# Performance work log

Hardware: AMD Instinct MI355X
Metric: run time of the kernel (lower is better)

The kernel has to match this reference:

```python
import jax, jax.numpy as jnp
import numpy as np

B, T, N, D = 4, 24, 5000, 64
M, K = 256, 20
TEMP = 0.5
MASK_T = int(T * 0.2)


def _random_walk(A):
    # D^-1 A with inf -> 0, as in calculate_random_walk_matrix
    deg = A.sum(axis=1)
    d_inv = jnp.where(deg > 0, 1.0 / deg, 0.0)
    return d_inv[:, None] * A


def _gnn(h, S1, S2, W, b):
    # SpatialConvOrderK, order=1, support_len=2, include_self=True
    # h: [B, C, N, T]; diffusion along node axis; 1x1 conv == channel matmul
    m1 = jnp.einsum('bcnt,mn->bcmt', h, S1)
    m2 = jnp.einsum('bcnt,mn->bcmt', h, S2)
    hc = jnp.concatenate([h, m1, m2], axis=1)  # [B, 3C, N, T]
    return jnp.einsum('bcnt,cd->bdnt', hc, W) + b[None, :, None, None]


def _encode(x, S1, S2, W_start, b_start, W1, b1, W2, b2):
    h = x @ W_start + b_start                 # [B, T, N, D]
    h = jnp.transpose(h, (0, 3, 2, 1))        # [B, D, N, T]
    h = jax.nn.relu(_gnn(h, S1, S2, W1, b1))
    h = _gnn(h, S1, S2, W2, b2)
    return h                                  # [B, D, N, T]


def _normalize(z):
    # cosine-similarity normalization over channel axis (dim=1), torch eps=1e-8
    n = jnp.sqrt(jnp.sum(z * z, axis=1, keepdims=True))
    return z / jnp.maximum(n, 1e-8)


def _forward(x, adj, W_start, b_start, W1, b1, W2, b2, Wf1, bf1, Wf2, bf2,
             missing_idx, pos_idx, neg_idx):
    S1 = _random_walk(adj)
    S2 = _random_walk(adj.T)
    h_ori = _encode(x, S1, S2, W_start, b_start, W1, b1, W2, b2)
    # augmented view: time-masked input through the same encoder
    x_aug = x.at[:, :MASK_T].set(0.0)
    h_aug = _encode(x_aug, S1, S2, W_start, b_start, W1, b1, W2, b2)
    # imputation head: final_linear1 -> relu -> final_linear2
    ht = jnp.transpose(h_ori, (0, 3, 2, 1))   # [B, T, N, D]
    y = jax.nn.relu(ht @ Wf1 + bf1) @ Wf2 + bf2  # [B, T, N, 1]
    # vectorized RSCL: batched gather + cosine sim + InfoNCE (label 0 = positive)
    Zo = _normalize(jnp.transpose(h_ori, (0, 1, 3, 2)))  # [B, D, T, N]
    Za = _normalize(jnp.transpose(h_aug, (0, 1, 3, 2)))
    anchor = Zo[..., missing_idx]             # [B, D, T, M]
    pos = Za[..., pos_idx]                    # [B, D, T, M]
    neg = Za[..., neg_idx]                    # [B, D, T, M, K]
    pos_sim = jnp.sum(anchor * pos, axis=1)                  # [B, T, M]
    neg_sim = jnp.einsum('bdtm,bdtmk->btmk', anchor, neg)    # [B, T, M, K]
    logits = jnp.concatenate([pos_sim[..., None], neg_sim], axis=-1) / TEMP
    # cross-entropy with label 0 == logsumexp - positive logit
    loss = jnp.mean(jax.nn.logsumexp(logits, axis=-1) - logits[..., 0])
    return y, loss


def setup_inputs() -> dict:
    key = jax.random.key(0)
    ks = jax.random.split(key, 12)
    x = jax.random.normal(ks[0], (B, T, N, 1), jnp.float32)
    adj = jax.random.uniform(ks[1], (N, N), jnp.float32)
    missing_idx = jax.random.randint(ks[2], (M,), 0, N)
    pos_idx = jax.random.randint(ks[3], (M,), 0, N)
    neg_idx = jax.random.randint(ks[4], (M, K), 0, N)
    s = lambda k, shp, fan: (jax.random.normal(k, shp, jnp.float32) / np.sqrt(fan)).astype(jnp.float32)
    W_start = s(ks[5], (1, D), 1.0)
    b_start = jnp.zeros((D,), jnp.float32)
    W1 = s(ks[6], (3 * D, D), 3.0 * D)
    b1 = jnp.zeros((D,), jnp.float32)
    W2 = s(ks[7], (3 * D, D), 3.0 * D)
    b2 = jnp.zeros((D,), jnp.float32)
    Wf1 = s(ks[8], (D, D // 2), float(D))
    bf1 = jnp.zeros((D // 2,), jnp.float32)
    Wf2 = s(ks[9], (D // 2, 1), float(D // 2))
    bf2 = jnp.zeros((1,), jnp.float32)
    return dict(x=x, adj=adj, W_start=W_start, b_start=b_start, W1=W1, b1=b1,
                W2=W2, b2=b2, Wf1=Wf1, bf1=bf1, Wf2=Wf2, bf2=bf2,
                missing_idx=missing_idx, pos_idx=pos_idx, neg_idx=neg_idx)


def reference(x, adj, W_start, b_start, W1, b1, W2, b2, Wf1, bf1, Wf2, bf2,
              missing_idx, pos_idx, neg_idx):
    return _forward(x, adj, W_start, b_start, W1, b1, W2, b2, Wf1, bf1, Wf2, bf2,
                    missing_idx, pos_idx, neg_idx)
```

## Files before the change

### kernel.cpp

```cpp
#include <hip/hip_runtime.h>

typedef unsigned char u8;
typedef unsigned short u16;
typedef unsigned int u32;
typedef __attribute__((ext_vector_type(8))) short short8;
typedef __attribute__((ext_vector_type(8))) u16 u16x8;
typedef __attribute__((ext_vector_type(4))) float f32x4;
typedef __attribute__((ext_vector_type(4))) int i32x4;
typedef __attribute__((ext_vector_type(8))) int i32x8;

#define N_NODES 5000
#define NP 5120
#define BTOT 96
#define J_DIM 6144
#define TT 24
#define KNEG 20

__device__ __forceinline__ float b2f(u16 u){ union{u32 i; float f;} x; x.i = ((u32)u)<<16; return x.f; }
__device__ __forceinline__ u16 f2b(float f){ union{float fl; u32 i;} x; x.fl = f; u32 r = (x.i + 0x7fffu + ((x.i>>16)&1u))>>16; return (u16)r; }
__device__ __forceinline__ u8 f2e4(float f){ return (u8)(__builtin_amdgcn_cvt_pk_fp8_f32(f, 0.f, 0, false) & 0xff); }

#define GPERM(r) ((((r)>>1)&3) | (((r)&1)<<2))
#define GLOAD16(g, l) __builtin_amdgcn_global_load_lds((const __attribute__((address_space(1))) void*)(g), (__attribute__((address_space(3))) void*)(l), 16, 0, 0)

__global__ void k_prep(const float* __restrict__ Ws, const float* __restrict__ bs,
                       const float* __restrict__ W1, const float* __restrict__ b1,
                       const float* __restrict__ W2, const float* __restrict__ b2,
                       float* __restrict__ consts, u16* __restrict__ w2t)
{
  int d = threadIdx.x;
  float u0=0.f,u1=0.f,u2=0.f,bb=0.f;
  for (int c=0;c<64;c++){
    float w = Ws[c];
    float a = W1[c*64+d], b_ = W1[(64+c)*64+d], cw = W1[(128+c)*64+d];
    u0 += w*a; u1 += w*b_; u2 += w*cw;
    bb += bs[c]*(a+b_+cw);
  }
  bb += b1[d];
  consts[d]=u0; consts[64+d]=u1; consts[128+d]=u2; consts[192+d]=bb;
  __shared__ float rb[64];
  rb[d] = fmaxf(bb, 0.f);
  __syncthreads();
  float cA=0.f,cB=0.f,cC=0.f;
  for (int c=0;c<64;c++){
    float r = rb[c];
    cA += r*W2[c*64+d]; cB += r*W2[(64+c)*64+d]; cC += r*W2[(128+c)*64+d];
  }
  consts[256+d]=cA; consts[320+d]=cB; consts[384+d]=cC;
  for (int c=0;c<192;c++) w2t[d*192 + c] = f2b(W2[c*64 + d]);
  __syncthreads();
  float b2v = b2[d];
  for (int vi=0; vi<4; vi++){
    float vv = cA + ((vi&1) ? cB : 0.f) + ((vi&2) ? cC : 0.f) + b2v;
    rb[d] = vv*vv;
    __syncthreads();
    for (int o=32;o;o>>=1){ if (d<o) rb[d]+=rb[d+o]; __syncthreads(); }
    float nrm = sqrtf(rb[0]);
    consts[448 + vi*64 + d] = vv / fmaxf(nrm, 1e-8f);
    __syncthreads();
  }
}

__global__ __launch_bounds__(256) void k_convT(const float* __restrict__ adj,
    u8* __restrict__ abf, u8* __restrict__ atbf,
    float* __restrict__ degr, float* __restrict__ degc)
{
  __shared__ u8 tN[64][80];
  __shared__ u8 tT[64][80];
  __shared__ float rsum[64];
  __shared__ float cpart[16][64];
  const int tid = threadIdx.x;
  const int bx = blockIdx.x, by = blockIdx.y;
  const int c4 = (tid & 15) * 4;
  const int g  = tid >> 4;
  const int gk = bx*64 + c4;
  float ca0=0.f, ca1=0.f, ca2=0.f, ca3=0.f;
  #pragma unroll
  for (int p=0;p<4;p++){
    int r = p*16 + g;
    int gm = by*64 + r;
    float v0=0.f,v1=0.f,v2=0.f,v3=0.f;
    if (gm < N_NODES && gk + 3 < N_NODES){
      const float4 v = *(const float4*)(adj + (size_t)gm*N_NODES + gk);
      v0=v.x; v1=v.y; v2=v.z; v3=v.w;
    }
    u8 p0=f2e4(v0), p1=f2e4(v1), p2=f2e4(v2), p3=f2e4(v3);
    *(u32*)&tN[r][c4] = (u32)p0 | ((u32)p1<<8) | ((u32)p2<<16) | ((u32)p3<<24);
    tT[c4+0][r]=p0; tT[c4+1][r]=p1; tT[c4+2][r]=p2; tT[c4+3][r]=p3;
    float ls = v0+v1+v2+v3;
    ls += __shfl_xor(ls,1); ls += __shfl_xor(ls,2);
    ls += __shfl_xor(ls,4); ls += __shfl_xor(ls,8);
    if ((tid & 15) == 0) rsum[r] = ls;
    ca0+=v0; ca1+=v1; ca2+=v2; ca3+=v3;
  }
  cpart[g][c4+0]=ca0; cpart[g][c4+1]=ca1; cpart[g][c4+2]=ca2; cpart[g][c4+3]=ca3;
  __syncthreads();
  if (tid < 64){
    int gm = by*64 + tid;
    if (gm < N_NODES && rsum[tid] != 0.f) atomicAdd(&degr[gm], rsum[tid]);
    float cs = 0.f;
    #pragma unroll
    for (int gg=0;gg<16;gg++) cs += cpart[gg][tid];
    int gc = bx*64 + tid;
    if (gc < N_NODES && cs != 0.f) atomicAdd(&degc[gc], cs);
  }
  const int j = tid >> 2, c16 = (tid & 3) * 16;
  *(i32x4*)(abf  + (size_t)(by*64+j)*NP + bx*64 + c16) = *(const i32x4*)(&tN[j][c16]);
  *(i32x4*)(atbf + (size_t)(bx*64+j)*NP + by*64 + c16) = *(const i32x4*)(&tT[j][c16]);
}

__global__ void k_xbf(const float* __restrict__ x, u8* __restrict__ xbf){
  int i4 = (blockIdx.x*256 + threadIdx.x)*4;
  int j = i4 / NP, n = i4 - j*NP;
  u32 w = 0;
  if (j < BTOT){
    #pragma unroll
    for (int e=0;e<4;e++){
      float v = (n+e < N_NODES) ? x[(size_t)j*N_NODES + n + e] : 0.f;
      w |= ((u32)f2e4(v)) << (8*e);
    }
  }
  *(u32*)(xbf + i4) = w;
}

__device__ __forceinline__ i32x8 frag8(const u8* lds, int row, int kb2){
  int g = GPERM(row & 7);
  int ba = row*128 + ((kb2 ^ g)<<4);
  union { i32x8 v; i32x4 h[2]; } f;
  f.h[0] = *(const i32x4*)(lds + ba);
  f.h[1] = *(const i32x4*)(lds + (ba^16));
  return f.v;
}

__global__ __launch_bounds__(256) void k_sgemm8(const u8* __restrict__ abf,
    const u8* __restrict__ atbf, const u8* __restrict__ B,
    float* __restrict__ y1sl, float* __restrict__ y2sl)
{
  __shared__ __align__(16) u8 lA[2][16384];
  __shared__ __align__(16) u8 lB[2][16384];
  const u8* A = blockIdx.z ? atbf : abf;
  float* ysl = blockIdx.z ? y2sl : y1sl;
  const int tid = threadIdx.x, lane = tid & 63, wv = tid >> 6;
  const int wm = (wv >> 1) * 64, wj = (wv & 1) * 64;
  const int m0 = blockIdx.x * 128;
  const int kbase = blockIdx.y * 640;
  f32x4 acc[4][4] = {};
  const int q = tid >> 3;
  const int sc = ((tid & 7) ^ GPERM(q & 7)) << 4;
  const u8* gA = A + (size_t)(m0 + q)*NP + kbase + sc;
  const u8* gB = B + (size_t)q*NP + kbase + sc;

  #define SSTAGE8(k0, bufA, bufB) do { \
    _Pragma("unroll") \
    for (int s=0;s<4;s++){ \
      GLOAD16(gA + (size_t)(s*32)*NP + (k0), (char*)(bufA) + s*4096 + wv*1024); \
      GLOAD16(gB + (size_t)(s*32)*NP + (k0), (char*)(bufB) + s*4096 + wv*1024); \
    } \
  } while(0)

  SSTAGE8(0,   lA[0], lB[0]);
  SSTAGE8(128, lA[1], lB[1]);
  asm volatile("s_waitcnt vmcnt(8)" ::: "memory");
  __builtin_amdgcn_s_barrier();
  __builtin_amdgcn_sched_barrier(0);

  for (int t = 0; t < 5; t++) {
    const int cur = t & 1;
    const u8* bA = lA[cur];
    const u8* bB = lB[cur];
    i32x8 af[4], bfv[4];
    const int kb2 = (lane >> 4) * 2;
    #pragma unroll
    for (int i=0;i<4;i++){
      af[i]  = frag8(bA, wm + i*16 + (lane&15), kb2);
      bfv[i] = frag8(bB, wj + i*16 + (lane&15), kb2);
    }
    __builtin_amdgcn_s_setprio(1);
    #pragma unroll
    for (int i=0;i<4;i++)
      #pragma unroll
      for (int j=0;j<4;j++)
        acc[i][j] = __builtin_amdgcn_mfma_scale_f32_16x16x128_f8f6f4(
            af[i], bfv[j], acc[i][j], 0, 0, 0, 0x7f7f7f7f, 0, 0x7f7f7f7f);
    __builtin_amdgcn_s_setprio(0);
    __builtin_amdgcn_s_barrier();
    __builtin_amdgcn_sched_barrier(0);
    if (t + 2 < 5) {
      SSTAGE8((t+2)*128, lA[cur], lB[cur]);
      asm volatile("s_waitcnt vmcnt(8)" ::: "memory");
    } else {
      asm volatile("s_waitcnt vmcnt(0)" ::: "memory");
    }
    __builtin_amdgcn_s_barrier();
    __builtin_amdgcn_sched_barrier(0);
  }
  #undef SSTAGE8

  float* yb = ysl + (size_t)blockIdx.y * NP * 128;
  #pragma unroll
  for (int i=0;i<4;i++)
    #pragma unroll
    for (int r=0;r<4;r++){
      int row = m0 + wm + i*16 + (lane>>4)*4 + r;
      #pragma unroll
      for (int j=0;j<4;j++){
        int col = wj + j*16 + (lane&15);
        yb[(size_t)row*128 + col] = acc[i][j][r];
      }
    }
}

__global__ __launch_bounds__(256) void k_yred(const float* __restrict__ y1sl,
    const float* __restrict__ y2sl, const float* __restrict__ degr,
    const float* __restrict__ degc, float* __restrict__ y1r, float* __restrict__ y2r)
{
  __shared__ float tb[128][66];
  const int n0 = blockIdx.x*64;
  const int bt = threadIdx.x & 127, nh = threadIdx.x >> 7;
  const int nl = threadIdx.x & 63, bh = threadIdx.x >> 6;
  #pragma unroll 4
  for (int k=0;k<32;k++){
    int n = nh*32 + k;
    float s = 0.f;
    #pragma unroll
    for (int sl=0; sl<8; sl++) s += y1sl[((size_t)sl*NP + n0+n)*128 + bt];
    tb[bt][n] = s;
  }
  __syncthreads();
  {
    float dv = degr[n0+nl];
    float iv = (dv > 0.f) ? 1.f/dv : 0.f;
    #pragma unroll 4
    for (int b=0;b<32;b++){
      int btw = bh*32 + b;
      y1r[(size_t)btw*NP + n0 + nl] = iv * tb[btw][nl];
    }
  }
  __syncthreads();
  #pragma unroll 4
  for (int k=0;k<32;k++){
    int n = nh*32 + k;
    float s = 0.f;
    #pragma unroll
    for (int sl=0; sl<8; sl++) s += y2sl[((size_t)sl*NP + n0+n)*128 + bt];
    tb[bt][n] = s;
  }
  __syncthreads();
  {
    float dv = degc[n0+nl];
    float iv = (dv > 0.f) ? 1.f/dv : 0.f;
    #pragma unroll 4
    for (int b=0;b<32;b++){
      int btw = bh*32 + b;
      y2r[(size_t)btw*NP + n0 + nl] = iv * tb[btw][nl];
    }
  }
}

__global__ __launch_bounds__(256) void k_h1(const float* __restrict__ x,
    const float* __restrict__ y1r, const float* __restrict__ y2r,
    const float* __restrict__ consts, u8* __restrict__ h1t, u16* __restrict__ h1n)
{
  __shared__ u8 trT[64][80];
  const int tid = threadIdx.x;
  const int n = tid & 63, d0 = (tid >> 6) * 16;
  const int n0 = blockIdx.x * 64;
  const int bt = blockIdx.y;
  const int gn = n0 + n;
  const bool valid = gn < N_NODES;
  float xv  = valid ? x[(size_t)bt*N_NODES + gn] : 0.f;
  float y1s = y1r[(size_t)bt*NP + gn];
  float y2s = y2r[(size_t)bt*NP + gn];
  float hv[16];
  #pragma unroll
  for (int e=0;e<16;e++){
    int d = d0 + e;
    float v = 0.f;
    if (valid)
      v = fmaxf(xv*consts[d] + y1s*consts[64+d] + y2s*consts[128+d] + consts[192+d], 0.f);
    hv[e] = v;
    trT[d][n] = f2e4(v);
  }
  u16x8 p0, p1;
  #pragma unroll
  for (int e=0;e<8;e++){ p0[e]=f2b(hv[e]); p1[e]=f2b(hv[8+e]); }
  u16* dst = h1n + (size_t)gn*J_DIM + bt*64 + d0;
  *(u16x8*)dst = p0;
  *(u16x8*)(dst+8) = p1;
  __syncthreads();
  const int d = tid >> 2, c16 = (tid & 3) * 16;
  *(i32x4*)(h1t + (size_t)(bt*64+d)*NP + n0 + c16) = *(const i32x4*)(&trT[d][c16]);
}

__global__ __launch_bounds__(512, 2) void k_gemm8(
    const u8* __restrict__ abf, const u8* __restrict__ atbf,
    const u8* __restrict__ Bt, u16* __restrict__ Pb, u16* __restrict__ Qb,
    const float* __restrict__ degr, const float* __restrict__ degc)
{
  __shared__ __align__(16) u8 lA[2][32768];
  __shared__ __align__(16) u8 lB[2][32768];
  const u8* A = blockIdx.z ? atbf : abf;
  u16* C = blockIdx.z ? Qb : Pb;
  const float* dg = blockIdx.z ? degc : degr;
  const int tid = threadIdx.x, lane = tid & 63, wv = tid >> 6;
  const int wm = (wv >> 1) * 64;
  const int wn = (wv & 1) * 128;
  const int m0 = blockIdx.x * 256;
  const int j0 = blockIdx.y * 256;
  f32x4 acc[4][8] = {};
  const int q = tid >> 3;
  const int sc = ((tid & 7) ^ GPERM(q & 7)) << 4;
  const u8* gA = A + (size_t)(m0 + q)*NP + sc;
  const u8* gB = Bt + (size_t)(j0 + q)*NP + sc;

  #define STAGE8(k0, bufA, bufB) do { \
    _Pragma("unroll") \
    for (int s=0;s<4;s++){ \
      GLOAD16(gA + (size_t)(s*64)*NP + (k0), (char*)(bufA) + s*8192 + wv*1024); \
      GLOAD16(gB + (size_t)(s*64)*NP + (k0), (char*)(bufB) + s*8192 + wv*1024); \
    } \
  } while(0)

  STAGE8(0,   lA[0], lB[0]);
  STAGE8(128, lA[1], lB[1]);
  asm volatile("s_waitcnt vmcnt(8)" ::: "memory");
  __builtin_amdgcn_s_barrier();
  __builtin_amdgcn_sched_barrier(0);

  const int NT = NP/128;
  for (int t = 0; t < NT; t++) {
    const int cur = t & 1;
    const u8* bA = lA[cur];
    const u8* bB = lB[cur];
    const int kb2 = (lane >> 4) * 2;
    const int rl = lane & 15;
    i32x8 af[4];
    #pragma unroll
    for (int i=0;i<4;i++) af[i] = frag8(bA, wm + i*16 + rl, kb2);
    __builtin_amdgcn_s_setprio(1);
    #pragma unroll
    for (int j=0;j<8;j++){
      i32x8 bf = frag8(bB, wn + j*16 + rl, kb2);
      #pragma unroll
      for (int i=0;i<4;i++)
        acc[i][j] = __builtin_amdgcn_mfma_scale_f32_16x16x128_f8f6f4(
            af[i], bf, acc[i][j], 0, 0, 0, 0x7f7f7f7f, 0, 0x7f7f7f7f);
    }
    __builtin_amdgcn_s_setprio(0);
    __builtin_amdgcn_s_barrier();
    __builtin_amdgcn_sched_barrier(0);
    if (t + 2 < NT) {
      STAGE8((t+2)*128, lA[cur], lB[cur]);
      asm volatile("s_waitcnt vmcnt(8)" ::: "memory");
    } else {
      asm volatile("s_waitcnt vmcnt(0)" ::: "memory");
    }
    __builtin_amdgcn_s_barrier();
    __builtin_amdgcn_sched_barrier(0);
  }
  #undef STAGE8

  #pragma unroll
  for (int i=0;i<4;i++)
    #pragma unroll
    for (int r=0;r<4;r++){
      int row = m0 + wm + i*16 + (lane>>4)*4 + r;
      float dv = dg[row];
      float scl = (dv > 0.f) ? 1.f/dv : 0.f;
      #pragma unroll
      for (int j=0;j<8;j++){
        int col = j0 + wn + j*16 + (lane&15);
        C[(size_t)row*J_DIM + col] = f2b(acc[i][j][r] * scl);
      }
    }
}

__global__ __launch_bounds__(256) void k_comb(const u16* __restrict__ h1n,
  const u16* __restrict__ P, const u16* __restrict__ Q,
  const u16* __restrict__ w2t, const float* __restrict__ b2,
  const float* __restrict__ Wf1, const float* __restrict__ bf1,
  const float* __restrict__ Wf2, const float* __restrict__ bf2,
  u16* __restrict__ horin, float* __restrict__ yout)
{
  __shared__ float w1L[64*33];
  __shared__ float hT[64][65];
  __shared__ float b1L[32], w2Ls[32];
  const int tid = threadIdx.x;
  for (int i = tid; i < 2048; i += 256) w1L[(i>>5)*33 + (i&31)] = Wf1[i];
  if (tid < 32){ b1L[tid] = bf1[tid]; w2Ls[tid] = Wf2[tid]; }
  const int lane = tid & 63;
  const int wv = tid >> 6;
  const int n0 = blockIdx.x * 64 + wv * 16;
  const int bt = blockIdx.y;
  const int rl = lane & 15, kh = lane >> 4;

  f32x4 acc[4] = {};
  const size_t rowoff = (size_t)(n0 + rl) * J_DIM + bt*64;
  const u16* bases[3] = { h1n + rowoff, P + rowoff, Q + rowoff };
  #pragma unroll
  for (int s=0;s<3;s++){
    const u16* base = bases[s];
    #pragma unroll
    for (int kk=0;kk<2;kk++){
      short8 af = *(const short8*)(base + kk*32 + kh*8);
      #pragma unroll
      for (int j=0;j<4;j++){
        short8 bf = *(const short8*)(w2t + (j*16+rl)*192 + s*64 + kk*32 + kh*8);
        acc[j] = __builtin_amdgcn_mfma_f32_16x16x32_bf16(af, bf, acc[j], 0,0,0);
      }
    }
  }
  float hvv[4][4];
  #pragma unroll
  for (int j=0;j<4;j++){
    float bias = b2[j*16 + rl];
    #pragma unroll
    for (int r=0;r<4;r++) hvv[j][r] = acc[j][r] + bias;
  }
  float inv[4];
  #pragma unroll
  for (int r=0;r<4;r++){
    float s = hvv[0][r]*hvv[0][r] + hvv[1][r]*hvv[1][r]
            + hvv[2][r]*hvv[2][r] + hvv[3][r]*hvv[3][r];
    s += __shfl_xor(s,1); s += __shfl_xor(s,2);
    s += __shfl_xor(s,4); s += __shfl_xor(s,8);
    inv[r] = 1.f / fmaxf(sqrtf(s), 1e-8f);
  }
  #pragma unroll
  for (int j=0;j<4;j++){
    int d = j*16 + rl;
    #pragma unroll
    for (int r=0;r<4;r++){
      int nn = n0 + kh*4 + r;
      hT[wv*16 + kh*4 + r][d] = hvv[j][r];
      if (nn < N_NODES)
        horin[((size_t)bt*N_NODES + nn)*64 + d] = f2b(hvv[j][r] * inv[r]);
    }
  }
  __syncthreads();
  const int qd = tid & 3, node = tid >> 2;
  float h[16];
  #pragma unroll
  for (int e=0;e<16;e++) h[e] = hT[node][qd*16 + e];
  float yacc = 0.f;
  #pragma unroll
  for (int jj=0; jj<32; jj++){
    float s = 0.f;
    #pragma unroll
    for (int dl=0; dl<16; dl++) s += h[dl]*w1L[(qd*16+dl)*33 + jj];
    s += __shfl_xor(s, 1);
    s += __shfl_xor(s, 2);
    s += b1L[jj];
    yacc += fmaxf(s, 0.f)*w2Ls[jj];
  }
  int gn = blockIdx.x*64 + node;
  if (qd == 0 && gn < N_NODES)
    yout[(size_t)bt*N_NODES + gn] = yacc + bf2[0];
}

__global__ __launch_bounds__(256) void k_loss(const u16* __restrict__ horin,
  const int* __restrict__ missing, const int* __restrict__ posi, const int* __restrict__ negi,
  const float* __restrict__ degr, const float* __restrict__ degc,
  const float* __restrict__ consts, float* __restrict__ out)
{
  const int lane = threadIdx.x & 63;
  const int wv = threadIdx.x >> 6;
  const int wg = blockIdx.x*4 + wv;
  const int m = wg & 255;
  const int bt = wg >> 8;
  const bool early = (bt % TT) < 4;

  int na = missing[m];
  float va = b2f(horin[((size_t)bt*N_NODES + na)*64 + lane]);

  float lk[KNEG+1];
  #pragma unroll
  for (int k=0;k<=KNEG;k++){
    int node = (k==0) ? posi[m] : negi[m*KNEG + (k-1)];
    float v;
    if (!early) v = b2f(horin[((size_t)bt*N_NODES + node)*64 + lane]);
    else {
      int vi = (degr[node] > 0.f ? 1 : 0) + (degc[node] > 0.f ? 2 : 0);
      v = consts[448 + vi*64 + lane];
    }
    float dp = va*v;
    #pragma unroll
    for (int o=32;o;o>>=1) dp += __shfl_xor(dp, o);
    lk[k] = dp * 2.f;
  }
  float mx = lk[0];
  #pragma unroll
  for (int k=1;k<=KNEG;k++) mx = fmaxf(mx, lk[k]);
  float se = 0.f;
  #pragma unroll
  for (int k=0;k<=KNEG;k++) se += expf(lk[k]-mx);
  float term = logf(se) + mx - lk[0];
  __shared__ float red[4];
  if (lane == 0) red[wv] = term;
  __syncthreads();
  if (threadIdx.x == 0)
    atomicAdd(out + 480000, (red[0]+red[1]+red[2]+red[3]) * (1.f/24576.f));
}

extern "C" void kernel_launch(void* const* d_in, const int* in_sizes, int n_in,
                              void* d_out, int out_size, void* d_ws, size_t ws_size,
                              hipStream_t stream)
{
  const float* x   = (const float*)d_in[0];
  const float* adj = (const float*)d_in[1];
  const float* Ws  = (const float*)d_in[2];
  const float* bs  = (const float*)d_in[3];
  const float* W1  = (const float*)d_in[4];
  const float* b1  = (const float*)d_in[5];
  const float* W2  = (const float*)d_in[6];
  const float* b2  = (const float*)d_in[7];
  const float* Wf1 = (const float*)d_in[8];
  const float* bf1 = (const float*)d_in[9];
  const float* Wf2 = (const float*)d_in[10];
  const float* bf2 = (const float*)d_in[11];
  const int* missing = (const int*)d_in[12];
  const int* posi    = (const int*)d_in[13];
  const int* negi    = (const int*)d_in[14];
  float* out = (float*)d_out;

  char* w = (char*)d_ws;
  u8*  abf   = (u8*) (w + 0);
  u8*  atbf  = (u8*) (w + 26214400);
  u8*  h1t   = (u8*) (w + 52428800);
  u16* h1n   = (u16*)(w + 83886080);
  u16* Pb    = (u16*)(w + 146800640);
  u16* Qb    = (u16*)(w + 209715200);
  u8*  xbf   = (u8*) (w + 272629760);
  float* degr = (float*)(w + 273285120);
  float* degc = (float*)(w + 273305600);
  float* consts = (float*)(w + 273326080);
  u16* w2t   = (u16*)(w + 273330176);
  u16*   horin = (u16*)(w + 0);
  float* y1sl  = (float*)(w + 146800640);
  float* y2sl  = (float*)(w + 167772160);
  float* y1r   = (float*)(w + 209715200);
  float* y2r   = (float*)(w + 212336640);

  hipMemsetAsync(degr, 0, 40960, stream);
  hipMemsetAsync(out + 480000, 0, 4, stream);

  k_prep<<<1, 64, 0, stream>>>(Ws, bs, W1, b1, W2, b2, consts, w2t);
  k_convT<<<dim3(80,80), 256, 0, stream>>>(adj, abf, atbf, degr, degc);
  k_xbf<<<640, 256, 0, stream>>>(x, xbf);
  k_sgemm8<<<dim3(40,8,2), 256, 0, stream>>>(abf, atbf, xbf, y1sl, y2sl);
  k_yred<<<80, 256, 0, stream>>>(y1sl, y2sl, degr, degc, y1r, y2r);
  k_h1<<<dim3(80,96), 256, 0, stream>>>(x, y1r, y2r, consts, h1t, h1n);
  k_gemm8<<<dim3(20,24,2), 512, 0, stream>>>(abf, atbf, h1t, Pb, Qb, degr, degc);
  k_comb<<<dim3(80,96), 256, 0, stream>>>(h1n, Pb, Qb, w2t, b2, Wf1, bf1, Wf2, bf2, horin, out);
  k_loss<<<6144, 256, 0, stream>>>(horin, missing, posi, negi, degr, degc, consts, out);
}
```

Before: 683.5 us.

## Shrink fp8 diffusion GEMM tiles to 128x128 with swizzled block order

Cuts the fp8 MFMA GEMM block tile from 256x256 with 512 threads to 128x128 with 256 threads, halving LDS per buffer and quadrupling the grid. It adds a block-index swizzle that spreads consecutive blocks across the grid, which may help L2 locality or spread work across XCDs. In k_h1 it remaps threads so each node's 16-channel segments sit in adjacent lanes, making the bf16 h1n stores more contiguous. Smaller tiles mean more redundant global loads of A and B per output but better occupancy and load balance.

Result: slower. 784.1 us (+14.7%).

```diff
diff --git a/kernel.cpp b/kernel.cpp
--- a/kernel.cpp
+++ b/kernel.cpp
@@ -263,7 +263,7 @@
 {
   __shared__ u8 trT[64][80];
   const int tid = threadIdx.x;
-  const int n = tid & 63, d0 = (tid >> 6) * 16;
+  const int n = tid >> 2, d0 = (tid & 3) * 16;
   const int n0 = blockIdx.x * 64;
   const int bt = blockIdx.y;
   const int gn = n0 + n;
@@ -292,22 +292,27 @@
   *(i32x4*)(h1t + (size_t)(bt*64+d)*NP + n0 + c16) = *(const i32x4*)(&trT[d][c16]);
 }
 
-__global__ __launch_bounds__(512, 2) void k_gemm8(
+__global__ __launch_bounds__(256) void k_gemm8(
     const u8* __restrict__ abf, const u8* __restrict__ atbf,
     const u8* __restrict__ Bt, u16* __restrict__ Pb, u16* __restrict__ Qb,
     const float* __restrict__ degr, const float* __restrict__ degc)
 {
-  __shared__ __align__(16) u8 lA[2][32768];
-  __shared__ __align__(16) u8 lB[2][32768];
-  const u8* A = blockIdx.z ? atbf : abf;
-  u16* C = blockIdx.z ? Qb : Pb;
-  const float* dg = blockIdx.z ? degc : degr;
+  __shared__ __align__(16) u8 lA[2][16384];
+  __shared__ __align__(16) u8 lB[2][16384];
+  const int lin = blockIdx.x + 40*blockIdx.y + 1920*blockIdx.z;
+  const int swz = (lin & 7)*480 + (lin >> 3);
+  const int bz = swz / 1920;
+  const int rem = swz - bz*1920;
+  const int byi = rem / 40;
+  const int bxi = rem - byi*40;
+  const u8* A = bz ? atbf : abf;
+  u16* C = bz ? Qb : Pb;
+  const float* dg = bz ? degc : degr;
   const int tid = threadIdx.x, lane = tid & 63, wv = tid >> 6;
-  const int wm = (wv >> 1) * 64;
-  const int wn = (wv & 1) * 128;
-  const int m0 = blockIdx.x * 256;
-  const int j0 = blockIdx.y * 256;
-  f32x4 acc[4][8] = {};
+  const int wm = (wv >> 1) * 64, wj = (wv & 1) * 64;
+  const int m0 = bxi * 128;
+  const int j0 = byi * 128;
+  f32x4 acc[4][4] = {};
   const int q = tid >> 3;
   const int sc = ((tid & 7) ^ GPERM(q & 7)) << 4;
   const u8* gA = A + (size_t)(m0 + q)*NP + sc;
@@ -316,8 +321,8 @@
   #define STAGE8(k0, bufA, bufB) do { \
     _Pragma("unroll") \
     for (int s=0;s<4;s++){ \
-      GLOAD16(gA + (size_t)(s*64)*NP + (k0), (char*)(bufA) + s*8192 + wv*1024); \
-      GLOAD16(gB + (size_t)(s*64)*NP + (k0), (char*)(bufB) + s*8192 + wv*1024); \
+      GLOAD16(gA + (size_t)(s*32)*NP + (k0), (char*)(bufA) + s*4096 + wv*1024); \
+      GLOAD16(gB + (size_t)(s*32)*NP + (k0), (char*)(bufB) + s*4096 + wv*1024); \
     } \
   } while(0)
 
@@ -332,20 +337,20 @@
     const int cur = t & 1;
     const u8* bA = lA[cur];
     const u8* bB = lB[cur];
+    i32x8 af[4], bfv[4];
     const int kb2 = (lane >> 4) * 2;
-    const int rl = lane & 15;
-    i32x8 af[4];
-    #pragma unroll
-    for (int i=0;i<4;i++) af[i] = frag8(bA, wm + i*16 + rl, kb2);
+    #pragma unroll
+    for (int i=0;i<4;i++){
+      af[i]  = frag8(bA, wm + i*16 + (lane&15), kb2);
+      bfv[i] = frag8(bB, wj + i*16 + (lane&15), kb2);
+    }
     __builtin_amdgcn_s_setprio(1);
     #pragma unroll
-    for (int j=0;j<8;j++){
-      i32x8 bf = frag8(bB, wn + j*16 + rl, kb2);
+    for (int i=0;i<4;i++)
       #pragma unroll
-      for (int i=0;i<4;i++)
+      for (int j=0;j<4;j++)
         acc[i][j] = __builtin_amdgcn_mfma_scale_f32_16x16x128_f8f6f4(
-            af[i], bf, acc[i][j], 0, 0, 0, 0x7f7f7f7f, 0, 0x7f7f7f7f);
-    }
+            af[i], bfv[j], acc[i][j], 0, 0, 0, 0x7f7f7f7f, 0, 0x7f7f7f7f);
     __builtin_amdgcn_s_setprio(0);
     __builtin_amdgcn_s_barrier();
     __builtin_amdgcn_sched_barrier(0);
@@ -368,8 +373,8 @@
       float dv = dg[row];
       float scl = (dv > 0.f) ? 1.f/dv : 0.f;
       #pragma unroll
-      for (int j=0;j<8;j++){
-        int col = j0 + wn + j*16 + (lane&15);
+      for (int j=0;j<4;j++){
+        int col = j0 + wj + j*16 + (lane&15);
         C[(size_t)row*J_DIM + col] = f2b(acc[i][j][r] * scl);
       }
     }
@@ -550,7 +555,7 @@
   k_sgemm8<<<dim3(40,8,2), 256, 0, stream>>>(abf, atbf, xbf, y1sl, y2sl);
   k_yred<<<80, 256, 0, stream>>>(y1sl, y2sl, degr, degc, y1r, y2r);
   k_h1<<<dim3(80,96), 256, 0, stream>>>(x, y1r, y2r, consts, h1t, h1n);
-  k_gemm8<<<dim3(20,24,2), 512, 0, stream>>>(abf, atbf, h1t, Pb, Qb, degr, degc);
+  k_gemm8<<<dim3(40,48,2), 256, 0, stream>>>(abf, atbf, h1t, Pb, Qb, degr, degc);
   k_comb<<<dim3(80,96), 256, 0, stream>>>(h1n, Pb, Qb, w2t, b2, Wf1, bf1, Wf2, bf2, horin, out);
   k_loss<<<6144, 256, 0, stream>>>(horin, missing, posi, negi, degr, degc, consts, out);
 }
```
